# Performance work log

Hardware: AMD Instinct MI355X
Metric: run time of the kernel (lower is better)

The kernel has to match this reference:

```python
import jax, jax.numpy as jnp
import numpy as np

EMBED_DIM = 1024
NUM_HEADS = 16
HEAD_DIM = EMBED_DIM // NUM_HEADS
SCALE = HEAD_DIM ** -0.5


def setup_inputs() -> dict:
    key = jax.random.key(0)
    ks = jax.random.split(key, 5)
    B, N, C = 4, 2048, EMBED_DIM
    s = C ** -0.5
    return {
        "x": jax.random.normal(ks[0], (B, N, C), dtype=jnp.float32),
        "w_qkv": jax.random.normal(ks[1], (C, 3 * C), dtype=jnp.float32) * s,
        "b_qkv": jnp.zeros((3 * C,), dtype=jnp.float32),
        "w_proj": jax.random.normal(ks[2], (C, C), dtype=jnp.float32) * s,
        "b_proj": jnp.zeros((C,), dtype=jnp.float32),
    }


def reference(x, w_qkv, b_qkv, w_proj, b_proj):
    B, N, C = x.shape
    H, D = NUM_HEADS, HEAD_DIM
    qkv = x @ w_qkv + b_qkv                      # (B, N, 3C)
    qkv = qkv.reshape(B, N, 3, H, D)
    qkv = jnp.transpose(qkv, (2, 0, 3, 1, 4))    # (3, B, H, N, D)
    q, k, v = qkv[0], qkv[1], qkv[2]
    attn = jnp.einsum('bhnd,bhmd->bhnm', q, k) * SCALE
    attn = jax.nn.softmax(attn, axis=-1)
    out = jnp.einsum('bhnm,bhmd->bhnd', attn, v)  # (B, H, N, D)
    out = jnp.transpose(out, (0, 2, 1, 3)).reshape(B, N, C)
    return out @ w_proj + b_proj
```

## Files before the change

kernel.cpp:

```cpp
#include <hip/hip_runtime.h>

typedef __attribute__((ext_vector_type(8))) short short8v;
typedef __attribute__((ext_vector_type(4))) short short4v;
typedef __attribute__((ext_vector_type(4))) float float4v;
typedef __attribute__((ext_vector_type(4))) unsigned short ushort4v;
typedef __attribute__((ext_vector_type(8))) unsigned short ushort8v;

#define GLOBAL_AS __attribute__((address_space(1)))
#define LDS_AS __attribute__((address_space(3)))

__device__ __forceinline__ void async_cp16(const void* g, void* l) {
  __builtin_amdgcn_global_load_lds((const GLOBAL_AS void*)g, (LDS_AS void*)l, 16, 0, 0);
}

__device__ __forceinline__ unsigned short f2bf(float f) {
  unsigned u = __float_as_uint(f);
  u += 0x7fffu + ((u >> 16) & 1u);
  return (unsigned short)(u >> 16);
}

#if defined(__HIP_DEVICE_COMPILE__)
#if __has_builtin(__builtin_amdgcn_mfma_f32_16x16x16bf16_1k)
#define MFMA_PV(a, b, c) __builtin_amdgcn_mfma_f32_16x16x16bf16_1k(a, b, c, 0, 0, 0)
#elif __has_builtin(__builtin_amdgcn_mfma_f32_16x16x16_bf16_1k)
#define MFMA_PV(a, b, c) __builtin_amdgcn_mfma_f32_16x16x16_bf16_1k(a, b, c, 0, 0, 0)
#elif __has_builtin(__builtin_amdgcn_mfma_f32_16x16x16_bf16)
#define MFMA_PV(a, b, c) __builtin_amdgcn_mfma_f32_16x16x16_bf16(a, b, c, 0, 0, 0)
#else
#error "no 16x16x16 bf16 mfma builtin on device"
#endif
#if __has_builtin(__builtin_amdgcn_exp2f)
#define EXP2F(x) __builtin_amdgcn_exp2f(x)
#else
#define EXP2F(x) exp2f(x)
#endif
#else
#define MFMA_PV(a, b, c) (c)
#define EXP2F(x) exp2f(x)
#endif

#if defined(__HIP_DEVICE_COMPILE__) && __has_builtin(__builtin_amdgcn_cvt_pk_bf16_f32)
typedef __attribute__((ext_vector_type(2))) __bf16 bf16x2v;
__device__ __forceinline__ unsigned pk_bf16(float a, float b) {
  bf16x2v r = __builtin_amdgcn_cvt_pk_bf16_f32(a, b);
  return __builtin_bit_cast(unsigned, r);
}
#else
__device__ __forceinline__ unsigned pk_bf16(float a, float b) {
  return (unsigned)f2bf(a) | ((unsigned)f2bf(b) << 16);
}
#endif

#define MFMA_QK(a, b, c) __builtin_amdgcn_mfma_f32_16x16x32_bf16(a, b, c, 0, 0, 0)


__global__ __launch_bounds__(256) void cvt_f32_bf16(const float* __restrict__ src,
                                                    unsigned short* __restrict__ dst) {
  int i = blockIdx.x * 256 + threadIdx.x;
  float4 v = ((const float4*)src)[i];
  ushort4v o;
  o.x = f2bf(v.x); o.y = f2bf(v.y); o.z = f2bf(v.z); o.w = f2bf(v.w);
  ((ushort4v*)dst)[i] = o;
}

__global__ __launch_bounds__(256) void transpose_w(const float* __restrict__ src,
                                                   unsigned short* __restrict__ dst,
                                                   int K, int N) {
  __shared__ float tile[64][65];
  int k0 = blockIdx.x * 64, n0 = blockIdx.y * 64;
  int t = threadIdx.x;
  int tc = t & 15, tr = t >> 4;
#pragma unroll
  for (int p = 0; p < 4; p++) {
    int r = tr + p * 16;
    float4 v = *(const float4*)(src + (size_t)(k0 + r) * N + n0 + tc * 4);
    tile[r][tc * 4 + 0] = v.x; tile[r][tc * 4 + 1] = v.y;
    tile[r][tc * 4 + 2] = v.z; tile[r][tc * 4 + 3] = v.w;
  }
  __syncthreads();
#pragma unroll
  for (int p = 0; p < 4; p++) {
    int rn = tr + p * 16;
    ushort4v o;
    o.x = f2bf(tile[tc * 4 + 0][rn]);
    o.y = f2bf(tile[tc * 4 + 1][rn]);
    o.z = f2bf(tile[tc * 4 + 2][rn]);
    o.w = f2bf(tile[tc * 4 + 3][rn]);
    *(ushort4v*)(dst + (size_t)(n0 + rn) * K + k0 + tc * 4) = o;
  }
}


__global__ __launch_bounds__(256) void gemm_qkv(const unsigned short* __restrict__ A,
                                                const unsigned short* __restrict__ BT,
                                                const float* __restrict__ bias,
                                                unsigned short* __restrict__ Qo,
                                                unsigned short* __restrict__ Ko,
                                                unsigned short* __restrict__ VTo) {
  __shared__ unsigned short As[128 * 32];
  __shared__ unsigned short Bs[128 * 32];
  int tid = threadIdx.x;
  int lane = tid & 63, w = tid >> 6, g = lane >> 4, c = lane & 15;
  int m0 = blockIdx.x * 128, n0 = blockIdx.y * 128;
  int wm = (w & 1) * 64, wn = (w >> 1) * 64;
  float4v acc[4][4] = {};

  for (int k0 = 0; k0 < 1024; k0 += 32) {
    __syncthreads();
#pragma unroll
    for (int p = 0; p < 2; p++) {
      int idx = p * 256 + tid;
      int row = idx >> 2, c8 = (idx & 3) * 8;
      async_cp16(A + (size_t)(m0 + row) * 1024 + k0 + c8, &As[idx * 8]);
      async_cp16(BT + (size_t)(n0 + row) * 1024 + k0 + c8, &Bs[idx * 8]);
    }
    __syncthreads();
    short8v af[4], bf[4];
#pragma unroll
    for (int i = 0; i < 4; i++)
      af[i] = *(const short8v*)(&As[(wm + i * 16 + c) * 32 + g * 8]);
#pragma unroll
    for (int j = 0; j < 4; j++)
      bf[j] = *(const short8v*)(&Bs[(wn + j * 16 + c) * 32 + g * 8]);
#pragma unroll
    for (int i = 0; i < 4; i++)
#pragma unroll
      for (int j = 0; j < 4; j++)
        acc[i][j] = MFMA_QK(af[i], bf[j], acc[i][j]);
  }

  int which = n0 >> 10;
#pragma unroll
  for (int j = 0; j < 4; j++) {
    int ng = n0 + wn + j * 16 + c;
    float bv = bias[ng];
    int h = (ng & 1023) >> 6, d = ng & 63;
#pragma unroll
    for (int i = 0; i < 4; i++) {
#pragma unroll
      for (int r = 0; r < 4; r++) {
        int mg = m0 + wm + i * 16 + g * 4 + r;
        int b = mg >> 11, n = mg & 2047;
        float v = acc[i][j][r] + bv;
        if (which == 0)
          Qo[((size_t)(b * 16 + h) * 2048 + n) * 64 + d] = f2bf(v * 0.18033688011112042f);
        else if (which == 1)
          Ko[((size_t)(b * 16 + h) * 2048 + n) * 64 + d] = f2bf(v);
        else
          VTo[((size_t)(b * 16 + h) * 64 + d) * 2048 + n] = f2bf(v);
      }
    }
  }
}


#define NTOK 2048
#define VTS 132

__global__ __launch_bounds__(256) void attn_kernel(const unsigned short* __restrict__ Qg,
                                                   const unsigned short* __restrict__ Kg,
                                                   const unsigned short* __restrict__ VTg,
                                                   unsigned short* __restrict__ Og) {
  __shared__ unsigned short Ks[128 * 64];
  __shared__ unsigned short VTsm[64 * VTS];

  int tid = threadIdx.x;
  int lane = tid & 63, w = tid >> 6, g = lane >> 4, c = lane & 15;
  int bh = blockIdx.y;
  int q0 = blockIdx.x * 128;

  const unsigned short* Qb = Qg + (size_t)bh * NTOK * 64;
  const unsigned short* Kb = Kg + (size_t)bh * NTOK * 64;
  const unsigned short* VTb = VTg + (size_t)bh * 64 * NTOK;

  short8v qf[2][2];
#pragma unroll
  for (int nt = 0; nt < 2; nt++)
#pragma unroll
    for (int kk = 0; kk < 2; kk++)
      qf[nt][kk] = *(const short8v*)(Qb + (size_t)(q0 + w * 32 + nt * 16 + c) * 64 +
                                     kk * 32 + g * 8);

  float4v L4[2] = {};
  float4v o[2][4] = {};

  for (int kt = 0; kt < NTOK; kt += 128) {
    __syncthreads();
#pragma unroll
    for (int p = 0; p < 4; p++) {
      int idx = p * 256 + tid;
      int row = idx >> 3, ch = idx & 7;
      async_cp16(Kb + (size_t)(kt + row) * 64 + ((ch ^ (row & 7)) * 8), &Ks[idx * 8]);
    }
    ushort8v vv[4];
    int vds[4], vcs[4];
#pragma unroll
    for (int p = 0; p < 4; p++) {
      int idx = p * 256 + tid;
      int d = idx >> 4, c8 = (idx & 15) * 8;
      vv[p] = *(const ushort8v*)(VTb + (size_t)d * NTOK + kt + c8);
      vds[p] = d; vcs[p] = c8;
    }
#pragma unroll
    for (int p = 0; p < 4; p++) {
      ushort4v lo = __builtin_shufflevector(vv[p], vv[p], 0, 1, 2, 3);
      ushort4v hi = __builtin_shufflevector(vv[p], vv[p], 4, 5, 6, 7);
      *(ushort4v*)(&VTsm[vds[p] * VTS + vcs[p]]) = lo;
      *(ushort4v*)(&VTsm[vds[p] * VTS + vcs[p] + 4]) = hi;
    }
    __syncthreads();

    float4v st[8][2] = {};
#pragma unroll
    for (int mt = 0; mt < 8; mt++) {
      int row = mt * 16 + c;
      short8v kf[2];
#pragma unroll
      for (int kk = 0; kk < 2; kk++) {
        int ch = (kk * 4 + g) ^ (row & 7);
        kf[kk] = *(const short8v*)(&Ks[row * 64 + ch * 8]);
      }
#pragma unroll
      for (int nt = 0; nt < 2; nt++)
#pragma unroll
        for (int kk = 0; kk < 2; kk++)
          st[mt][nt] = MFMA_QK(kf[kk], qf[nt][kk], st[mt][nt]);
    }

#pragma unroll
    for (int nt = 0; nt < 2; nt++)
#pragma unroll
      for (int mt = 0; mt < 8; mt++) {
        float4v s4 = st[mt][nt];
        s4.x = EXP2F(s4.x); s4.y = EXP2F(s4.y);
        s4.z = EXP2F(s4.z); s4.w = EXP2F(s4.w);
        st[mt][nt] = s4;
        L4[nt] += s4;
      }

#pragma unroll
    for (int kk8 = 0; kk8 < 8; kk8++) {
      short4v pa[2];
#pragma unroll
      for (int nt = 0; nt < 2; nt++) {
        float4v p4 = st[kk8][nt];
        union { unsigned u[2]; short4v s; } cv;
        cv.u[0] = pk_bf16(p4.x, p4.y);
        cv.u[1] = pk_bf16(p4.z, p4.w);
        pa[nt] = cv.s;
      }
#pragma unroll
      for (int nt_o = 0; nt_o < 4; nt_o++) {
        short4v vb = *(const short4v*)(&VTsm[(nt_o * 16 + c) * VTS + kk8 * 16 + g * 4]);
#pragma unroll
        for (int mt_o = 0; mt_o < 2; mt_o++)
          o[mt_o][nt_o] = MFMA_PV(pa[mt_o], vb, o[mt_o][nt_o]);
      }
    }
  }

  float L[2];
#pragma unroll
  for (int nt = 0; nt < 2; nt++) {
    float l = L4[nt].x + L4[nt].y + L4[nt].z + L4[nt].w;
    l += __shfl_xor(l, 16);
    l += __shfl_xor(l, 32);
    L[nt] = l;
  }
  int b = bh >> 4, h = bh & 15;
#pragma unroll
  for (int mt_o = 0; mt_o < 2; mt_o++) {
    float4v li;
#pragma unroll
    for (int r = 0; r < 4; r++) li[r] = 1.0f / __shfl(L[mt_o], g * 4 + r);
#pragma unroll
    for (int nt_o = 0; nt_o < 4; nt_o++) {
      float4v v = o[mt_o][nt_o] * li;
      int col = h * 64 + nt_o * 16 + c;
      int rowbase = b * NTOK + q0 + w * 32 + mt_o * 16 + g * 4;
#pragma unroll
      for (int r = 0; r < 4; r++)
        Og[(size_t)(rowbase + r) * 1024 + col] = f2bf(v[r]);
    }
  }
}

__global__ __launch_bounds__(256) void gemm_proj(const unsigned short* __restrict__ A,
                                                 const unsigned short* __restrict__ BT,
                                                 const float* __restrict__ bias,
                                                 float* __restrict__ out) {
  __shared__ unsigned short As[128 * 32];
  __shared__ unsigned short Bs[128 * 32];
  int tid = threadIdx.x;
  int lane = tid & 63, w = tid >> 6, g = lane >> 4, c = lane & 15;
  int m0 = blockIdx.x * 128, n0 = blockIdx.y * 128;
  int wm = (w & 1) * 64, wn = (w >> 1) * 64;
  float4v acc[4][4] = {};

  for (int k0 = 0; k0 < 1024; k0 += 32) {
    __syncthreads();
#pragma unroll
    for (int p = 0; p < 2; p++) {
      int idx = p * 256 + tid;
      int row = idx >> 2, c8 = (idx & 3) * 8;
      async_cp16(A + (size_t)(m0 + row) * 1024 + k0 + c8, &As[idx * 8]);
      async_cp16(BT + (size_t)(n0 + row) * 1024 + k0 + c8, &Bs[idx * 8]);
    }
    __syncthreads();
    short8v af[4], bf[4];
#pragma unroll
    for (int i = 0; i < 4; i++)
      af[i] = *(const short8v*)(&As[(wm + i * 16 + c) * 32 + g * 8]);
#pragma unroll
    for (int j = 0; j < 4; j++)
      bf[j] = *(const short8v*)(&Bs[(wn + j * 16 + c) * 32 + g * 8]);
#pragma unroll
    for (int i = 0; i < 4; i++)
#pragma unroll
      for (int j = 0; j < 4; j++)
        acc[i][j] = MFMA_QK(af[i], bf[j], acc[i][j]);
  }

#pragma unroll
  for (int j = 0; j < 4; j++) {
    int ng = n0 + wn + j * 16 + c;
    float bv = bias[ng];
#pragma unroll
    for (int i = 0; i < 4; i++) {
#pragma unroll
      for (int r = 0; r < 4; r++) {
        int mg = m0 + wm + i * 16 + g * 4 + r;
        out[(size_t)mg * 1024 + ng] = acc[i][j][r] + bv;
      }
    }
  }
}


extern "C" void kernel_launch(void* const* d_in, const int* in_sizes, int n_in,
                              void* d_out, int out_size, void* d_ws, size_t ws_size,
                              hipStream_t stream) {
  (void)in_sizes; (void)n_in; (void)out_size; (void)ws_size;
  const float* x = (const float*)d_in[0];
  const float* w_qkv = (const float*)d_in[1];
  const float* b_qkv = (const float*)d_in[2];
  const float* w_proj = (const float*)d_in[3];
  const float* b_proj = (const float*)d_in[4];
  float* out = (float*)d_out;

  unsigned short* x_bf = (unsigned short*)d_ws;
  unsigned short* wqkvT = x_bf + (size_t)8192 * 1024;
  unsigned short* wprojT = wqkvT + (size_t)3072 * 1024;
  unsigned short* qws = wprojT + (size_t)1024 * 1024;
  unsigned short* kws = qws + (size_t)8388608;
  unsigned short* vtws = kws + (size_t)8388608;
  unsigned short* aws = vtws + (size_t)8388608;

  cvt_f32_bf16<<<8192, 256, 0, stream>>>(x, x_bf);
  transpose_w<<<dim3(16, 48), 256, 0, stream>>>(w_qkv, wqkvT, 1024, 3072);
  transpose_w<<<dim3(16, 16), 256, 0, stream>>>(w_proj, wprojT, 1024, 1024);
  gemm_qkv<<<dim3(64, 24), 256, 0, stream>>>(x_bf, wqkvT, b_qkv, qws, kws, vtws);
  attn_kernel<<<dim3(16, 64), 256, 0, stream>>>(qws, kws, vtws, aws);
  gemm_proj<<<dim3(64, 8), 256, 0, stream>>>(aws, wprojT, b_proj, out);
}
```

Before: 303.6 us.

## Async-load swizzled V tiles, compute softmax denominator via MFMA, shrink proj GEMM tile

The attention kernel now loads the transposed V tile straight into LDS with async global-to-LDS copies using an XOR swizzle, in place of register staging into a padded array. Exponentiation is moved into the PV loop. The row-sum denominator is now accumulated with an extra MFMA against a vector of bf16 ones, which removes the scalar adds and cross-lane shuffles. Separately, the projection GEMM uses 64-row M tiles and doubles its grid, aiming for better occupancy and load balance at the cost of less data reuse per block.

```diff
diff --git a/kernel.cpp b/kernel.cpp
--- a/kernel.cpp
+++ b/kernel.cpp
@@ -155,17 +155,17 @@
 
 
 #define NTOK 2048
-#define VTS 132
 
 __global__ __launch_bounds__(256) void attn_kernel(const unsigned short* __restrict__ Qg,
                                                    const unsigned short* __restrict__ Kg,
                                                    const unsigned short* __restrict__ VTg,
                                                    unsigned short* __restrict__ Og) {
   __shared__ unsigned short Ks[128 * 64];
-  __shared__ unsigned short VTsm[64 * VTS];
+  __shared__ unsigned short VTs[64 * 128];
 
   int tid = threadIdx.x;
   int lane = tid & 63, w = tid >> 6, g = lane >> 4, c = lane & 15;
+  int gh = g >> 1, g1 = g & 1;
   int bh = blockIdx.y;
   int q0 = blockIdx.x * 128;
 
@@ -181,7 +181,11 @@
       qf[nt][kk] = *(const short8v*)(Qb + (size_t)(q0 + w * 32 + nt * 16 + c) * 64 +
                                      kk * 32 + g * 8);
 
-  float4v L4[2] = {};
+  short4v ones;
+  ones.x = (short)0x3F80; ones.y = (short)0x3F80;
+  ones.z = (short)0x3F80; ones.w = (short)0x3F80;
+
+  float4v lacc[2] = {};
   float4v o[2][4] = {};
 
   for (int kt = 0; kt < NTOK; kt += 128) {
@@ -192,21 +196,11 @@
       int row = idx >> 3, ch = idx & 7;
       async_cp16(Kb + (size_t)(kt + row) * 64 + ((ch ^ (row & 7)) * 8), &Ks[idx * 8]);
     }
-    ushort8v vv[4];
-    int vds[4], vcs[4];
 #pragma unroll
     for (int p = 0; p < 4; p++) {
       int idx = p * 256 + tid;
-      int d = idx >> 4, c8 = (idx & 15) * 8;
-      vv[p] = *(const ushort8v*)(VTb + (size_t)d * NTOK + kt + c8);
-      vds[p] = d; vcs[p] = c8;
-    }
-#pragma unroll
-    for (int p = 0; p < 4; p++) {
-      ushort4v lo = __builtin_shufflevector(vv[p], vv[p], 0, 1, 2, 3);
-      ushort4v hi = __builtin_shufflevector(vv[p], vv[p], 4, 5, 6, 7);
-      *(ushort4v*)(&VTsm[vds[p] * VTS + vcs[p]]) = lo;
-      *(ushort4v*)(&VTsm[vds[p] * VTS + vcs[p] + 4]) = hi;
+      int d = idx >> 4, ch = idx & 15;
+      async_cp16(VTb + (size_t)d * NTOK + kt + ((ch ^ (d & 15)) * 8), &VTs[idx * 8]);
     }
     __syncthreads();
 
@@ -228,51 +222,39 @@
     }
 
 #pragma unroll
-    for (int nt = 0; nt < 2; nt++)
-#pragma unroll
-      for (int mt = 0; mt < 8; mt++) {
-        float4v s4 = st[mt][nt];
-        s4.x = EXP2F(s4.x); s4.y = EXP2F(s4.y);
-        s4.z = EXP2F(s4.z); s4.w = EXP2F(s4.w);
-        st[mt][nt] = s4;
-        L4[nt] += s4;
-      }
-
-#pragma unroll
     for (int kk8 = 0; kk8 < 8; kk8++) {
       short4v pa[2];
 #pragma unroll
       for (int nt = 0; nt < 2; nt++) {
         float4v p4 = st[kk8][nt];
+        p4.x = EXP2F(p4.x); p4.y = EXP2F(p4.y);
+        p4.z = EXP2F(p4.z); p4.w = EXP2F(p4.w);
         union { unsigned u[2]; short4v s; } cv;
         cv.u[0] = pk_bf16(p4.x, p4.y);
         cv.u[1] = pk_bf16(p4.z, p4.w);
         pa[nt] = cv.s;
       }
+      int pc = (kk8 * 2 + gh) ^ c;
+      const unsigned short* vp = &VTs[c * 128 + pc * 8 + g1 * 4];
 #pragma unroll
       for (int nt_o = 0; nt_o < 4; nt_o++) {
-        short4v vb = *(const short4v*)(&VTsm[(nt_o * 16 + c) * VTS + kk8 * 16 + g * 4]);
+        short4v vb = *(const short4v*)(vp + nt_o * 16 * 128);
 #pragma unroll
         for (int mt_o = 0; mt_o < 2; mt_o++)
           o[mt_o][nt_o] = MFMA_PV(pa[mt_o], vb, o[mt_o][nt_o]);
       }
-    }
-  }
-
-  float L[2];
-#pragma unroll
-  for (int nt = 0; nt < 2; nt++) {
-    float l = L4[nt].x + L4[nt].y + L4[nt].z + L4[nt].w;
-    l += __shfl_xor(l, 16);
-    l += __shfl_xor(l, 32);
-    L[nt] = l;
-  }
+#pragma unroll
+      for (int mt_o = 0; mt_o < 2; mt_o++)
+        lacc[mt_o] = MFMA_PV(pa[mt_o], ones, lacc[mt_o]);
+    }
+  }
+
   int b = bh >> 4, h = bh & 15;
 #pragma unroll
   for (int mt_o = 0; mt_o < 2; mt_o++) {
     float4v li;
 #pragma unroll
-    for (int r = 0; r < 4; r++) li[r] = 1.0f / __shfl(L[mt_o], g * 4 + r);
+    for (int r = 0; r < 4; r++) li[r] = 1.0f / lacc[mt_o][r];
 #pragma unroll
     for (int nt_o = 0; nt_o < 4; nt_o++) {
       float4v v = o[mt_o][nt_o] * li;
@@ -285,37 +267,41 @@
   }
 }
 
+
 __global__ __launch_bounds__(256) void gemm_proj(const unsigned short* __restrict__ A,
                                                  const unsigned short* __restrict__ BT,
                                                  const float* __restrict__ bias,
                                                  float* __restrict__ out) {
-  __shared__ unsigned short As[128 * 32];
+  __shared__ unsigned short As[64 * 32];
   __shared__ unsigned short Bs[128 * 32];
   int tid = threadIdx.x;
   int lane = tid & 63, w = tid >> 6, g = lane >> 4, c = lane & 15;
-  int m0 = blockIdx.x * 128, n0 = blockIdx.y * 128;
-  int wm = (w & 1) * 64, wn = (w >> 1) * 64;
-  float4v acc[4][4] = {};
+  int m0 = blockIdx.x * 64, n0 = blockIdx.y * 128;
+  int wm = (w & 1) * 32, wn = (w >> 1) * 64;
+  float4v acc[2][4] = {};
 
   for (int k0 = 0; k0 < 1024; k0 += 32) {
     __syncthreads();
+    {
+      int row = tid >> 2, c8 = (tid & 3) * 8;
+      async_cp16(A + (size_t)(m0 + row) * 1024 + k0 + c8, &As[tid * 8]);
+    }
 #pragma unroll
     for (int p = 0; p < 2; p++) {
       int idx = p * 256 + tid;
       int row = idx >> 2, c8 = (idx & 3) * 8;
-      async_cp16(A + (size_t)(m0 + row) * 1024 + k0 + c8, &As[idx * 8]);
       async_cp16(BT + (size_t)(n0 + row) * 1024 + k0 + c8, &Bs[idx * 8]);
     }
     __syncthreads();
-    short8v af[4], bf[4];
-#pragma unroll
-    for (int i = 0; i < 4; i++)
+    short8v af[2], bf[4];
+#pragma unroll
+    for (int i = 0; i < 2; i++)
       af[i] = *(const short8v*)(&As[(wm + i * 16 + c) * 32 + g * 8]);
 #pragma unroll
     for (int j = 0; j < 4; j++)
       bf[j] = *(const short8v*)(&Bs[(wn + j * 16 + c) * 32 + g * 8]);
 #pragma unroll
-    for (int i = 0; i < 4; i++)
+    for (int i = 0; i < 2; i++)
 #pragma unroll
       for (int j = 0; j < 4; j++)
         acc[i][j] = MFMA_QK(af[i], bf[j], acc[i][j]);
@@ -326,7 +312,7 @@
     int ng = n0 + wn + j * 16 + c;
     float bv = bias[ng];
 #pragma unroll
-    for (int i = 0; i < 4; i++) {
+    for (int i = 0; i < 2; i++) {
 #pragma unroll
       for (int r = 0; r < 4; r++) {
         int mg = m0 + wm + i * 16 + g * 4 + r;
@@ -361,5 +347,5 @@
   transpose_w<<<dim3(16, 16), 256, 0, stream>>>(w_proj, wprojT, 1024, 1024);
   gemm_qkv<<<dim3(64, 24), 256, 0, stream>>>(x_bf, wqkvT, b_qkv, qws, kws, vtws);
   attn_kernel<<<dim3(16, 64), 256, 0, stream>>>(qws, kws, vtws, aws);
-  gemm_proj<<<dim3(64, 8), 256, 0, stream>>>(aws, wprojT, b_proj, out);
-}
+  gemm_proj<<<dim3(128, 8), 256, 0, stream>>>(aws, wprojT, b_proj, out);
+}
```

New measurement: 323.6 us. 6.6% more time.
